# Kernel tuning notes

Hardware: AMD Instinct MI355X
Metric: run time of the kernel (lower is better)

## Reference

```python
import jax, jax.numpy as jnp
import numpy as np

B, T, C, H, D, K = 2, 2048, 1024, 16, 64, 4
INNER = H * D
EPS = 1e-6


def l2_norm(x):
    return x * jax.lax.rsqrt(jnp.sum(x * x, axis=-1, keepdims=True) + EPS)


def rms_norm(x):
    return x * jax.lax.rsqrt(jnp.mean(x * x, axis=-1, keepdims=True) + EPS)


def conv_silu(x, w, b):
    # causal depthwise conv1d + SiLU; x: [B,T,inner], w: [inner,1,K], b: [inner]
    xc = jnp.transpose(x, (0, 2, 1))
    xc = jnp.pad(xc, ((0, 0), (0, 0), (K - 1, 0)))
    xc = jax.lax.conv_general_dilated(
        xc, w.astype(xc.dtype), window_strides=(1,), padding='VALID',
        dimension_numbers=('NCW', 'OIW', 'NCW'), feature_group_count=xc.shape[1])
    xc = xc + b.astype(xc.dtype)[:, None]
    return jnp.transpose(jax.nn.silu(xc), (0, 2, 1))


def setup_inputs() -> dict:
    key = jax.random.key(0)
    ks = jax.random.split(key, 16)

    def lin(k, o, i):
        return jax.random.normal(k, (o, i), jnp.float32) / np.float32(np.sqrt(i))

    dt_min, dt_max = 0.001, 0.1
    dt = jnp.exp(jax.random.uniform(ks[12], (H,)) * (np.log(dt_max) - np.log(dt_min)) + np.log(dt_min))
    return {
        'x': jax.random.normal(ks[0], (B, T, C), jnp.float32),
        'wq': lin(ks[1], INNER, C), 'wk': lin(ks[2], INNER, C),
        'wv': lin(ks[3], INNER, C), 'wg': lin(ks[4], INNER, C),
        'wo': lin(ks[5], C, INNER),
        'wa': lin(ks[6], H, C), 'wb': lin(ks[7], H, C),
        'conv_q_w': jax.random.normal(ks[8], (INNER, 1, K)) * 0.02, 'conv_q_b': jnp.zeros(INNER),
        'conv_k_w': jax.random.normal(ks[9], (INNER, 1, K)) * 0.02, 'conv_k_b': jnp.zeros(INNER),
        'conv_v_w': jax.random.normal(ks[10], (INNER, 1, K)) * 0.02, 'conv_v_b': jnp.zeros(INNER),
        'A_log': jnp.log(jax.random.uniform(ks[11], (H,), minval=0.0, maxval=16.0) + 1e-6),
        'dt_bias': dt + jnp.log(-jnp.expm1(-dt)),
        'o_norm_scale': jnp.ones(D),
    }


def reference(x, wq, wk, wv, wg, wo, wa, wb,
              conv_q_w, conv_q_b, conv_k_w, conv_k_b, conv_v_w, conv_v_b,
              A_log, dt_bias, o_norm_scale):
    q = conv_silu(x @ wq.T, conv_q_w, conv_q_b).reshape(B, T, H, D)
    k = conv_silu(x @ wk.T, conv_k_w, conv_k_b).reshape(B, T, H, D)
    v = conv_silu(x @ wv.T, conv_v_w, conv_v_b).reshape(B, T, H, D)
    g_out = (x @ wg.T).reshape(B, T, H, D)

    q = l2_norm(q)
    k = l2_norm(k)

    beta = jax.nn.sigmoid(x @ wb.T)                     # [B,T,H]
    a = x @ wa.T + dt_bias                              # [B,T,H]
    decay = jnp.exp(-jnp.exp(A_log) * jax.nn.softplus(a))

    # time-major for scan
    q_T = jnp.transpose(q, (1, 0, 2, 3))
    k_T = jnp.transpose(k, (1, 0, 2, 3))
    v_T = jnp.transpose(v, (1, 0, 2, 3))
    beta_T = jnp.transpose(beta, (1, 0, 2))
    decay_T = jnp.transpose(decay, (1, 0, 2))

    def step(S_prev, xs):
        q_t, k_t, v_t, beta_t, decay_t = xs
        kS = jnp.einsum('bhd,bhde->bhe', k_t, S_prev)
        delta = v_t - kS
        write = beta_t[..., None, None] * jnp.einsum('bhd,bhe->bhde', k_t, delta)
        S_new = decay_t[..., None, None] * S_prev + write
        o_t = jnp.einsum('bhd,bhde->bhe', q_t, S_new)
        return S_new, o_t

    S_init = jnp.zeros((B, H, D, D), dtype=x.dtype)
    _, o_T = jax.lax.scan(step, S_init, (q_T, k_T, v_T, beta_T, decay_T))

    o = jnp.transpose(o_T, (1, 0, 2, 3))                # [B,T,H,D]
    o = rms_norm(o) * o_norm_scale
    o = o * jax.nn.silu(g_out)
    return o.reshape(B, T, INNER) @ wo.T
```

## Files before the change

### kernel.cpp

```cpp
#include <hip/hip_runtime.h>
#include <math.h>

#define BB 2
#define TT 2048
#define CC 1024
#define HH 16
#define DD 64
#define INNER 1024
#define BT (BB*TT)
#define EPSF 1e-6f
#define CH 64
#define NC (TT/CH)
#define NBH (BB*HH)
#define NCHK (NBH*NC)

typedef unsigned short u16;
typedef __bf16 bf16x8 __attribute__((ext_vector_type(8)));
typedef float f32x4 __attribute__((ext_vector_type(4)));

__device__ inline u16 f2bf(float f) {
  unsigned u = __builtin_bit_cast(unsigned, f);
  return (u16)((u + 0x7fffu + ((u >> 16) & 1u)) >> 16);
}
__device__ inline float b2f(u16 b) {
  unsigned u = ((unsigned)b) << 16;
  return __builtin_bit_cast(float, u);
}
__device__ inline void gll16(const u16* g, u16* l) {
  __builtin_amdgcn_global_load_lds(
      (const __attribute__((address_space(1))) void*)g,
      (__attribute__((address_space(3))) void*)l, 16, 0, 0);
}

__device__ u16   g_pqb[BT * INNER];
__device__ u16   g_pkb[BT * INNER];
__device__ u16   g_pvb[BT * INNER];
__device__ u16   g_qb [BT * INNER];
__device__ u16   g_kb [BT * INNER];
__device__ u16   g_vb [BT * INNER];
__device__ u16   g_gb [BT * INNER];
__device__ u16   g_ob [BT * INNER];
__device__ float g_beta[BT * HH];
__device__ float g_ldec[BT * HH];
__device__ u16   g_xb[BT * CC];
__device__ u16   g_wbb[4 * INNER * CC];
__device__ u16   g_wob[CC * INNER];
__device__ u16   g_gatedb[BT * INNER];
__device__ u16   g_U0 [NCHK * CH * DD];
__device__ u16   g_Wt [NCHK * DD * CH];
__device__ u16   g_Bt [NCHK * CH * CH];
__device__ u16   g_Qht[NCHK * DD * CH];
__device__ float g_Mc [NCHK * DD * DD];
__device__ float g_bc [NCHK * DD * DD];
__device__ float g_Sall[NCHK * DD * DD];

__global__ __launch_bounds__(256) void cast_all(
    const float* __restrict__ x, const float* __restrict__ wq,
    const float* __restrict__ wk, const float* __restrict__ wv,
    const float* __restrict__ wg, const float* __restrict__ wo,
    u16* __restrict__ xb, u16* __restrict__ wb, u16* __restrict__ wob) {
  long i = ((long)blockIdx.x * 256 + threadIdx.x) * 4;
  const float* src;
  u16* dst;
  if (i < 4194304)      { src = x  + i;             dst = xb + i; }
  else if (i < 5242880) { src = wq + (i - 4194304); dst = wb + (i - 4194304); }
  else if (i < 6291456) { src = wk + (i - 5242880); dst = wb + (i - 4194304); }
  else if (i < 7340032) { src = wv + (i - 6291456); dst = wb + (i - 4194304); }
  else if (i < 8388608) { src = wg + (i - 7340032); dst = wb + (i - 4194304); }
  else                  { src = wo + (i - 8388608); dst = wob + (i - 8388608); }
  float4 v = *(const float4*)src;
  ushort4 o;
  o.x = f2bf(v.x); o.y = f2bf(v.y); o.z = f2bf(v.z); o.w = f2bf(v.w);
  *(ushort4*)dst = o;
}

template <typename OutT, int NBN>
__global__ __launch_bounds__(256) void bgemm4(
    const u16* __restrict__ A, const u16* __restrict__ B,
    OutT* __restrict__ c0, OutT* __restrict__ c1,
    OutT* __restrict__ c2, OutT* __restrict__ c3) {
  __shared__ u16 lA[128 * 64];
  __shared__ u16 lB[128 * 64];
  const int tid = threadIdx.x;
  const int bid = blockIdx.x;
  int bm, bn;
  if constexpr (NBN == 32) {
    const int xcd = bid & 7;
    const int idx = bid >> 3;
    const int in_ = idx >> 4;
    int im = idx & 15;
    im = (in_ & 1) ? (15 - im) : im;
    bm = ((xcd >> 2) * 16 + im) * 128;
    bn = ((xcd & 3) * 8 + in_) * 128;
  } else {
    const int xcd = bid & 7;
    const int idx = bid >> 3;
    const int in_ = idx >> 2;
    int im = idx & 3;
    im = (in_ & 1) ? (3 - im) : im;
    bm = (xcd * 4 + im) * 128;
    bn = in_ * 128;
  }
  const int lane = tid & 63;
  const int wave = tid >> 6;
  const int wr = (wave >> 1) * 64, wc = (wave & 1) * 64;
  const int lr = lane & 15;
  const int kq = lane >> 4;
  const int srow0 = tid >> 3;
  const int gcol = ((tid & 7) ^ (srow0 & 7)) * 8;
  const u16* gA0 = &A[(long)(bm + srow0) * CC + gcol];
  const u16* gB0 = &B[(long)(bn + srow0) * CC + gcol];
  u16* lA0 = &lA[tid * 8];
  u16* lB0 = &lB[tid * 8];
  f32x4 acc[4][4] = {};

  for (int k0 = 0; k0 < CC; k0 += 64) {
    __syncthreads();
#pragma unroll
    for (int p = 0; p < 4; ++p) {
      gll16(gA0 + (long)p * 32 * CC + k0, lA0 + p * 2048);
      gll16(gB0 + (long)p * 32 * CC + k0, lB0 + p * 2048);
    }
    __syncthreads();
#pragma unroll
    for (int ks = 0; ks < 2; ++ks) {
      const int sl = ((ks * 4 + kq) ^ (lr & 7)) * 8;
      bf16x8 af[4], bf_[4];
#pragma unroll
      for (int m = 0; m < 4; ++m)
        af[m] = __builtin_bit_cast(bf16x8,
            *(const uint4*)&lA[(wr + m * 16 + lr) * 64 + sl]);
#pragma unroll
      for (int n = 0; n < 4; ++n)
        bf_[n] = __builtin_bit_cast(bf16x8,
            *(const uint4*)&lB[(wc + n * 16 + lr) * 64 + sl]);
#pragma unroll
      for (int m = 0; m < 4; ++m)
#pragma unroll
        for (int n = 0; n < 4; ++n)
          acc[m][n] = __builtin_amdgcn_mfma_f32_16x16x32_bf16(
              af[m], bf_[n], acc[m][n], 0, 0, 0);
    }
  }
  OutT* cp = (bn < 1024) ? c0 : (bn < 2048) ? c1 : (bn < 3072) ? c2 : c3;
  const int ccol0 = (bn & 1023) + wc;
  const int crow0 = bm + wr + kq * 4;
#pragma unroll
  for (int m = 0; m < 4; ++m)
#pragma unroll
    for (int n = 0; n < 4; ++n) {
      int col = ccol0 + n * 16 + lr;
#pragma unroll
      for (int r = 0; r < 4; ++r) {
        long idx2 = (long)(crow0 + m * 16 + r) * INNER + col;
        if constexpr (sizeof(OutT) == 2) cp[idx2] = f2bf(acc[m][n][r]);
        else                             cp[idx2] = acc[m][n][r];
      }
    }
}

__global__ __launch_bounds__(256) void conv3(
    const u16* __restrict__ pq, const u16* __restrict__ pk,
    const u16* __restrict__ pv,
    const float* __restrict__ cqw, const float* __restrict__ cqb,
    const float* __restrict__ ckw, const float* __restrict__ ckb,
    const float* __restrict__ cvw, const float* __restrict__ cvb,
    u16* __restrict__ oq, u16* __restrict__ ok, u16* __restrict__ ov) {
  const int which = blockIdx.y;
  const u16* pre = which == 0 ? pq : which == 1 ? pk : pv;
  const float* cw = which == 0 ? cqw : which == 1 ? ckw : cvw;
  const float* cb = which == 0 ? cqb : which == 1 ? ckb : cvb;
  u16* out = which == 0 ? oq : which == 1 ? ok : ov;
  const int do_l2 = (which < 2);

  const int bt = blockIdx.x;
  const int b = bt / TT, t = bt % TT;
  const int tid = threadIdx.x;
  const int c4 = tid * 4;
  float xt[4][4];
#pragma unroll
  for (int j = 0; j < 4; ++j) {
    int ts = t - 3 + j;
    if (ts >= 0) {
      ushort4 u = *(const ushort4*)&pre[(long)(b * TT + ts) * INNER + c4];
      xt[j][0] = b2f(u.x); xt[j][1] = b2f(u.y);
      xt[j][2] = b2f(u.z); xt[j][3] = b2f(u.w);
    } else {
      xt[j][0] = xt[j][1] = xt[j][2] = xt[j][3] = 0.f;
    }
  }
  float4 bias4 = *(const float4*)&cb[c4];
  const float* bp = (const float*)&bias4;
  float y[4];
#pragma unroll
  for (int ci = 0; ci < 4; ++ci) {
    float4 w4 = *(const float4*)&cw[(c4 + ci) * 4];
    float acc = bp[ci];
    acc += w4.x * xt[0][ci];
    acc += w4.y * xt[1][ci];
    acc += w4.z * xt[2][ci];
    acc += w4.w * xt[3][ci];
    y[ci] = acc / (1.f + expf(-acc));
  }
  if (do_l2) {
    float ssq = y[0]*y[0] + y[1]*y[1] + y[2]*y[2] + y[3]*y[3];
    ssq += __shfl_xor(ssq, 1);
    ssq += __shfl_xor(ssq, 2);
    ssq += __shfl_xor(ssq, 4);
    ssq += __shfl_xor(ssq, 8);
    float r = rsqrtf(ssq + EPSF);
    y[0] *= r; y[1] *= r; y[2] *= r; y[3] *= r;
  }
  ushort4 res;
  res.x = f2bf(y[0]); res.y = f2bf(y[1]);
  res.z = f2bf(y[2]); res.w = f2bf(y[3]);
  *(ushort4*)&out[(long)bt * INNER + c4] = res;
}

__global__ __launch_bounds__(256) void proj_ab3(
    const float* __restrict__ x, const float* __restrict__ wa,
    const float* __restrict__ wb, const float* __restrict__ dt_bias,
    const float* __restrict__ A_log, float* __restrict__ beta,
    float* __restrict__ ldec) {
  const int m0 = blockIdx.x * 8;
  const int tid = threadIdx.x;
  __shared__ float xs[8][132];
  __shared__ float ws[32][132];
  const int row = tid >> 5;
  const int col = tid & 31;
  float a0 = 0.f, a1 = 0.f, a2 = 0.f, a3 = 0.f;
  const int sxr = tid >> 5, sxc = (tid & 31) * 4;
  for (int k0 = 0; k0 < CC; k0 += 128) {
    __syncthreads();
    *(float4*)&xs[sxr][sxc] = *(const float4*)&x[(long)(m0 + sxr) * CC + k0 + sxc];
#pragma unroll
    for (int p = 0; p < 4; ++p) {
      int idx = tid + p * 256;
      int wr = idx >> 5, wc4 = (idx & 31) * 4;
      const float* wsrc = (wr < 16) ? &wa[(long)wr * CC] : &wb[(long)(wr - 16) * CC];
      *(float4*)&ws[wr][wc4] = *(const float4*)&wsrc[k0 + wc4];
    }
    __syncthreads();
#pragma unroll
    for (int kk = 0; kk < 128; kk += 16) {
      float4 x0 = *(const float4*)&xs[row][kk + 0];
      float4 w0 = *(const float4*)&ws[col][kk + 0];
      float4 x1 = *(const float4*)&xs[row][kk + 4];
      float4 w1 = *(const float4*)&ws[col][kk + 4];
      float4 x2 = *(const float4*)&xs[row][kk + 8];
      float4 w2 = *(const float4*)&ws[col][kk + 8];
      float4 x3 = *(const float4*)&xs[row][kk + 12];
      float4 w3 = *(const float4*)&ws[col][kk + 12];
      a0 += x0.x * w0.x + x0.y * w0.y + x0.z * w0.z + x0.w * w0.w;
      a1 += x1.x * w1.x + x1.y * w1.y + x1.z * w1.z + x1.w * w1.w;
      a2 += x2.x * w2.x + x2.y * w2.y + x2.z * w2.z + x2.w * w2.w;
      a3 += x3.x * w3.x + x3.y * w3.y + x3.z * w3.z + x3.w * w3.w;
    }
  }
  float acc = (a0 + a1) + (a2 + a3);
  const int m = m0 + row;
  if (col < 16) {
    float a = acc + dt_bias[col];
    float sp = fmaxf(a, 0.f) + log1pf(expf(-fabsf(a)));
    ldec[(long)m * HH + col] = -expf(A_log[col]) * sp;
  } else {
    beta[(long)m * HH + (col - 16)] = 1.f / (1.f + expf(-acc));
  }
}

__global__ __launch_bounds__(256) void gdn_prep(
    const u16* __restrict__ q, const u16* __restrict__ k,
    const u16* __restrict__ v, const float* __restrict__ beta,
    const float* __restrict__ ldec,
    u16* __restrict__ U0g, u16* __restrict__ Wtg, u16* __restrict__ Btg,
    u16* __restrict__ Qhtg, float* __restrict__ Mtg, float* __restrict__ bvg) {
  const int blk = blockIdx.x;
  const int bh = blk / NC, c = blk % NC;
  const int b = bh >> 4, h = bh & 15;
  const int tid = threadIdx.x;
  const int tx = tid & 15, ty = tid >> 4;
  __shared__ float P0[64][68];
  __shared__ float P1[64][68];
  __shared__ float Ab[64][68];
  __shared__ float lam[64], lamx[64], lbet[64];
  const long gb = ((long)(b * TT + c * CH) * HH + h) * DD;

  {
    const int e4 = (tid & 15) * 4;
    const int t0 = tid >> 4;
#pragma unroll
    for (int p = 0; p < 4; ++p) {
      int t = t0 + p * 16;
      ushort4 qv = *(const ushort4*)&q[gb + (long)t * (HH * DD) + e4];
      P1[e4 + 0][t] = b2f(qv.x); P1[e4 + 1][t] = b2f(qv.y);
      P1[e4 + 2][t] = b2f(qv.z); P1[e4 + 3][t] = b2f(qv.w);
    }
  }
  float ldv = 0.f, bv_ = 0.f;
  if (tid < 64) {
    ldv = ldec[(long)(b * TT + c * CH + tid) * HH + h];
    bv_ = beta[(long)(b * TT + c * CH + tid) * HH + h];
    lam[tid] = ldv;
  }
  __syncthreads();
  float lsum = 0.f;
  if (tid < 64) {
    for (int s = 0; s <= tid; ++s) lsum += lam[s];
  }
  __syncthreads();
  if (tid < 64) {
    lam[tid] = lsum;
    lamx[tid] = lsum - ldv;
    lbet[tid] = bv_;
  }
  __syncthreads();

  {
    const int lane = tid & 63;
    const int wave = tid >> 6;
    const int lr = lane & 15;
    const int kq = lane >> 4;
    const int mwr = (wave >> 1) * 32, mwc = (wave & 1) * 32;
    bf16x8 af[2][2], bk_[2][2], bq_[2][2];
#pragma unroll
    for (int m = 0; m < 2; ++m)
#pragma unroll
      for (int ks = 0; ks < 2; ++ks) {
        long rbase = gb + (long)(mwr + m * 16 + lr) * (HH * DD) + ks * 32 + kq * 8;
        long cbase = gb + (long)(mwc + m * 16 + lr) * (HH * DD) + ks * 32 + kq * 8;
        af[m][ks]  = __builtin_bit_cast(bf16x8, *(const uint4*)&k[rbase]);
        bk_[m][ks] = __builtin_bit_cast(bf16x8, *(const uint4*)&k[cbase]);
        bq_[m][ks] = __builtin_bit_cast(bf16x8, *(const uint4*)&q[cbase]);
      }
    f32x4 gf[2][2] = {}, pf[2][2] = {};
#pragma unroll
    for (int ks = 0; ks < 2; ++ks)
#pragma unroll
      for (int m = 0; m < 2; ++m)
#pragma unroll
        for (int n = 0; n < 2; ++n) {
          gf[m][n] = __builtin_amdgcn_mfma_f32_16x16x32_bf16(
              af[m][ks], bk_[n][ks], gf[m][n], 0, 0, 0);
          pf[m][n] = __builtin_amdgcn_mfma_f32_16x16x32_bf16(
              af[m][ks], bq_[n][ks], pf[m][n], 0, 0, 0);
        }
    u16* btp = Btg + (long)blk * (CH * CH);
#pragma unroll
    for (int m = 0; m < 2; ++m)
#pragma unroll
      for (int n = 0; n < 2; ++n)
#pragma unroll
        for (int r = 0; r < 4; ++r) {
          int t = mwr + m * 16 + kq * 4 + r;
          int s = mwc + n * 16 + lr;
          Ab[t][s] = (s < t) ? lbet[t] * expf(lamx[t] - lam[s]) * gf[m][n][r]
                             : 0.f;
          btp[t * 64 + s] = f2bf(
              (t <= s) ? expf(lam[s] - lam[t]) * pf[m][n][r] : 0.f);
        }
  }
  {
    u16* qhp = Qhtg + (long)blk * (DD * CH);
    const int t4 = (tid & 15) * 4;
    const int d0 = tid >> 4;
#pragma unroll
    for (int p = 0; p < 4; ++p) {
      int d = d0 + p * 16;
      float4 qv = *(const float4*)&P1[d][t4];
      ushort4 qw;
      qw.x = f2bf(qv.x * expf(lam[t4 + 0]));
      qw.y = f2bf(qv.y * expf(lam[t4 + 1]));
      qw.z = f2bf(qv.z * expf(lam[t4 + 2]));
      qw.w = f2bf(qv.w * expf(lam[t4 + 3]));
      *(ushort4*)&qhp[d * 64 + t4] = qw;
    }
  }
  __syncthreads();
  {
    const int e4 = (tid & 15) * 4;
    const int t0 = tid >> 4;
#pragma unroll
    for (int p = 0; p < 4; ++p) {
      int t = t0 + p * 16;
      float bt_ = lbet[t], cx = bt_ * expf(lamx[t]);
      ushort4 vv4 = *(const ushort4*)&v[gb + (long)t * (HH * DD) + e4];
      ushort4 kv4 = *(const ushort4*)&k[gb + (long)t * (HH * DD) + e4];
      float4 vv = make_float4(b2f(vv4.x) * bt_, b2f(vv4.y) * bt_,
                              b2f(vv4.z) * bt_, b2f(vv4.w) * bt_);
      float4 kv = make_float4(b2f(kv4.x) * cx, b2f(kv4.y) * cx,
                              b2f(kv4.z) * cx, b2f(kv4.w) * cx);
      *(float4*)&P0[t][e4] = vv;
      *(float4*)&P1[t][e4] = kv;
    }
  }
  __syncthreads();
  {
    const int i = tid >> 5;
    const int j4 = (tid & 31) * 4;
    float* Pj = (j4 < 64) ? (&P0[0][0] + j4) : (&P1[0][0] + (j4 - 64));
#pragma unroll
    for (int base = 0; base < 64; base += 8) {
      const int r = base + i;
      float4 acc = *(const float4*)&Pj[r * 68];
      for (int t = 0; t < base; ++t) {
        float a = Ab[r][t];
        float4 ut = *(const float4*)&Pj[t * 68];
        acc.x -= a * ut.x; acc.y -= a * ut.y;
        acc.z -= a * ut.z; acc.w -= a * ut.w;
      }
      *(float4*)&Pj[r * 68] = acc;
      __syncthreads();
      float4 val[8];
#pragma unroll
      for (int t = 0; t < 8; ++t) {
        float4 vt = *(const float4*)&Pj[(base + t) * 68];
#pragma unroll
        for (int m = 0; m < t; ++m) {
          float a = Ab[base + t][base + m];
          vt.x -= a * val[m].x; vt.y -= a * val[m].y;
          vt.z -= a * val[m].z; vt.w -= a * val[m].w;
        }
        val[t] = vt;
      }
      float4 fin = val[0];
#pragma unroll
      for (int t = 1; t < 8; ++t) if (i == t) fin = val[t];
      __syncthreads();
      *(float4*)&Pj[r * 68] = fin;
      __syncthreads();
    }
  }
  {
    u16* u0p = U0g + (long)blk * (CH * DD);
    const int e4 = (tid & 15) * 4;
    const int t0 = tid >> 4;
    float lamL = lam[63];
#pragma unroll
    for (int p = 0; p < 4; ++p) {
      int t = t0 + p * 16;
      float4 u4 = *(const float4*)&P0[t][e4];
      ushort4 uw;
      uw.x = f2bf(u4.x); uw.y = f2bf(u4.y);
      uw.z = f2bf(u4.z); uw.w = f2bf(u4.w);
      *(ushort4*)&u0p[t * 64 + e4] = uw;
      float cf = expf(lamL - lam[t]);
      ushort4 kv4 = *(const ushort4*)&k[gb + (long)t * (HH * DD) + e4];
      *(float4*)&Ab[t][e4] = make_float4(b2f(kv4.x) * cf, b2f(kv4.y) * cf,
                                         b2f(kv4.z) * cf, b2f(kv4.w) * cf);
    }
    u16* wtp = Wtg + (long)blk * (DD * CH);
    const int t = tid & 63;
    const int d0 = tid >> 6;
#pragma unroll
    for (int p = 0; p < 16; ++p) {
      int d = d0 + p * 4;
      wtp[d * 64 + t] = f2bf(P1[t][d]);
    }
  }
  __syncthreads();
  {
    float accm[4][4] = {}, accb[4][4] = {};
    for (int t = 0; t < 64; ++t) {
      float4 ka = *(const float4*)&Ab[t][ty * 4];
      float4 wc_ = *(const float4*)&P1[t][tx * 4];
      float4 uv = *(const float4*)&P0[t][tx * 4];
      float kar[4] = {ka.x, ka.y, ka.z, ka.w};
      float wcr[4] = {wc_.x, wc_.y, wc_.z, wc_.w};
      float ucr[4] = {uv.x, uv.y, uv.z, uv.w};
#pragma unroll
      for (int i = 0; i < 4; ++i)
#pragma unroll
        for (int j = 0; j < 4; ++j) {
          accm[i][j] += kar[i] * wcr[j];
          accb[i][j] += kar[i] * ucr[j];
        }
    }
    float gLv = expf(lam[63]);
    float* mp = Mtg + (long)blk * (DD * DD);
    float* bp = bvg + (long)blk * (DD * DD);
#pragma unroll
    for (int i = 0; i < 4; ++i) {
      int rr = ty * 4 + i;
      float4 mv, b4;
      mv.x = ((rr == tx * 4 + 0) ? gLv : 0.f) - accm[i][0];
      mv.y = ((rr == tx * 4 + 1) ? gLv : 0.f) - accm[i][1];
      mv.z = ((rr == tx * 4 + 2) ? gLv : 0.f) - accm[i][2];
      mv.w = ((rr == tx * 4 + 3) ? gLv : 0.f) - accm[i][3];
      *(float4*)&mp[rr * 64 + tx * 4] = mv;
      b4.x = accb[i][0]; b4.y = accb[i][1];
      b4.z = accb[i][2]; b4.w = accb[i][3];
      *(float4*)&bp[rr * 64 + tx * 4] = b4;
    }
  }
}

__global__ __launch_bounds__(256) void gdn_seq5(
    const float* __restrict__ Mtg, const float* __restrict__ bvg,
    float* __restrict__ Sall) {
  const int bh = blockIdx.x & 31;
  const int esec = blockIdx.x >> 5;
  const int tid = threadIdx.x;
  const int lane = tid & 63;
  const int w = tid >> 6;
  const int d = w * 16 + (lane & 15);
  const int q = lane >> 4;
  const int eo = esec * 4;
  __shared__ float Ss[4][68];
  float S0 = 0.f, S1 = 0.f, S2 = 0.f, S3 = 0.f;
  float4 mreg[4], mnext[4];
  float4 breg, bnext;
  {
    const float* mt0 = Mtg + (long)bh * NC * 4096;
#pragma unroll
    for (int p = 0; p < 4; ++p)
      mreg[p] = *(const float4*)&mt0[d * 64 + q * 16 + p * 4];
    breg = *(const float4*)&bvg[(long)bh * NC * 4096 + d * 64 + eo];
  }
  for (int c = 0; c < NC; ++c) {
    const long cb = (long)bh * NC + c;
    if (q == 0) {
      *(float4*)&Sall[cb * 4096 + d * 64 + eo] = make_float4(S0, S1, S2, S3);
      Ss[0][d] = S0; Ss[1][d] = S1; Ss[2][d] = S2; Ss[3][d] = S3;
    }
    __syncthreads();
    if (c + 1 < NC) {
      const float* mtn = Mtg + (cb + 1) * 4096;
#pragma unroll
      for (int p = 0; p < 4; ++p)
        mnext[p] = *(const float4*)&mtn[d * 64 + q * 16 + p * 4];
      bnext = *(const float4*)&bvg[(cb + 1) * 4096 + d * 64 + eo];
    }
    float p0 = 0.f, p1 = 0.f, p2 = 0.f, p3 = 0.f;
#pragma unroll
    for (int j = 0; j < 4; ++j) {
      float4 m4 = mreg[j];
      float4 s0 = *(const float4*)&Ss[0][q * 16 + j * 4];
      float4 s1 = *(const float4*)&Ss[1][q * 16 + j * 4];
      float4 s2 = *(const float4*)&Ss[2][q * 16 + j * 4];
      float4 s3 = *(const float4*)&Ss[3][q * 16 + j * 4];
      p0 += m4.x * s0.x + m4.y * s0.y + m4.z * s0.z + m4.w * s0.w;
      p1 += m4.x * s1.x + m4.y * s1.y + m4.z * s1.z + m4.w * s1.w;
      p2 += m4.x * s2.x + m4.y * s2.y + m4.z * s2.z + m4.w * s2.w;
      p3 += m4.x * s3.x + m4.y * s3.y + m4.z * s3.z + m4.w * s3.w;
    }
    p0 += __shfl_xor(p0, 16); p0 += __shfl_xor(p0, 32);
    p1 += __shfl_xor(p1, 16); p1 += __shfl_xor(p1, 32);
    p2 += __shfl_xor(p2, 16); p2 += __shfl_xor(p2, 32);
    p3 += __shfl_xor(p3, 16); p3 += __shfl_xor(p3, 32);
    S0 = breg.x + p0; S1 = breg.y + p1;
    S2 = breg.z + p2; S3 = breg.w + p3;
    __syncthreads();
    mreg[0] = mnext[0]; mreg[1] = mnext[1];
    mreg[2] = mnext[2]; mreg[3] = mnext[3];
    breg = bnext;
  }
}

__global__ __launch_bounds__(256) void gdn_out(
    const u16* __restrict__ U0g, const u16* __restrict__ Wtg,
    const u16* __restrict__ Btg, const u16* __restrict__ Qhtg,
    const float* __restrict__ Sall, u16* __restrict__ o) {
  const int blk = blockIdx.x;
  const int bh = blk / NC, c = blk % NC;
  const int b = bh >> 4, h = bh & 15;
  const int tid = threadIdx.x;
  const int tx = tid & 15, ty = tid >> 4;
  __shared__ float S[64][64];
  __shared__ float ub[64][64];
  __shared__ float op[64][64];
  const int e4 = (tid & 15) * 4;
  const int t0s = tid >> 4;
  {
    const int r = tid >> 2, qq = (tid & 3) * 16;
#pragma unroll
    for (int p = 0; p < 4; ++p)
      *(float4*)&S[r][qq + p * 4] =
          *(const float4*)&Sall[(long)blk * 4096 + r * 64 + qq + p * 4];
  }
#pragma unroll
  for (int p = 0; p < 4; ++p) {
    int t = t0s + p * 16;
    ushort4 w4 = *(const ushort4*)&Wtg[(long)blk * 4096 + t * 64 + e4];
    *(float4*)&op[t][e4] = make_float4(b2f(w4.x), b2f(w4.y), b2f(w4.z), b2f(w4.w));
  }
  __syncthreads();
  float acc[4][4];
#pragma unroll
  for (int i = 0; i < 4; ++i) {
    ushort4 u4 = *(const ushort4*)&U0g[(long)blk * 4096 + (ty * 4 + i) * 64 + tx * 4];
    acc[i][0] = b2f(u4.x); acc[i][1] = b2f(u4.y);
    acc[i][2] = b2f(u4.z); acc[i][3] = b2f(u4.w);
  }
  for (int d = 0; d < 64; ++d) {
    float4 a4 = *(const float4*)&op[d][ty * 4];
    float4 b4 = *(const float4*)&S[d][tx * 4];
    float ar[4] = {a4.x, a4.y, a4.z, a4.w};
    float br[4] = {b4.x, b4.y, b4.z, b4.w};
#pragma unroll
    for (int i = 0; i < 4; ++i)
#pragma unroll
      for (int j = 0; j < 4; ++j) acc[i][j] -= ar[i] * br[j];
  }
#pragma unroll
  for (int i = 0; i < 4; ++i)
    *(float4*)&ub[ty * 4 + i][tx * 4] =
        make_float4(acc[i][0], acc[i][1], acc[i][2], acc[i][3]);
  __syncthreads();
#pragma unroll
  for (int p = 0; p < 4; ++p) {
    int t = t0s + p * 16;
    ushort4 w4 = *(const ushort4*)&Btg[(long)blk * 4096 + t * 64 + e4];
    *(float4*)&op[t][e4] = make_float4(b2f(w4.x), b2f(w4.y), b2f(w4.z), b2f(w4.w));
  }
  __syncthreads();
  float acco[4][4] = {};
  for (int s = 0; s < 64; ++s) {
    float4 a4 = *(const float4*)&op[s][ty * 4];
    float4 b4 = *(const float4*)&ub[s][tx * 4];
    float ar[4] = {a4.x, a4.y, a4.z, a4.w};
    float br[4] = {b4.x, b4.y, b4.z, b4.w};
#pragma unroll
    for (int i = 0; i < 4; ++i)
#pragma unroll
      for (int j = 0; j < 4; ++j) acco[i][j] += ar[i] * br[j];
  }
  __syncthreads();
#pragma unroll
  for (int p = 0; p < 4; ++p) {
    int t = t0s + p * 16;
    ushort4 w4 = *(const ushort4*)&Qhtg[(long)blk * 4096 + t * 64 + e4];
    *(float4*)&op[t][e4] = make_float4(b2f(w4.x), b2f(w4.y), b2f(w4.z), b2f(w4.w));
  }
  __syncthreads();
  for (int d = 0; d < 64; ++d) {
    float4 a4 = *(const float4*)&op[d][ty * 4];
    float4 b4 = *(const float4*)&S[d][tx * 4];
    float ar[4] = {a4.x, a4.y, a4.z, a4.w};
    float br[4] = {b4.x, b4.y, b4.z, b4.w};
#pragma unroll
    for (int i = 0; i < 4; ++i)
#pragma unroll
      for (int j = 0; j < 4; ++j) acco[i][j] += ar[i] * br[j];
  }
#pragma unroll
  for (int i = 0; i < 4; ++i) {
    int t = ty * 4 + i;
    ushort4 ow;
    ow.x = f2bf(acco[i][0]); ow.y = f2bf(acco[i][1]);
    ow.z = f2bf(acco[i][2]); ow.w = f2bf(acco[i][3]);
    *(ushort4*)&o[((long)(b * TT + c * CH + t) * HH + h) * DD + tx * 4] = ow;
  }
}

__global__ __launch_bounds__(256) void norm_gate(
    const u16* __restrict__ o, const u16* __restrict__ g,
    const float* __restrict__ scale, u16* __restrict__ outb) {
  const int bt = blockIdx.x;
  const int tid = threadIdx.x;
  const int c4 = tid * 4;
  ushort4 o4u = *(const ushort4*)&o[(long)bt * INNER + c4];
  float4 o4 = make_float4(b2f(o4u.x), b2f(o4u.y), b2f(o4u.z), b2f(o4u.w));
  float ssq = o4.x * o4.x + o4.y * o4.y + o4.z * o4.z + o4.w * o4.w;
  ssq += __shfl_xor(ssq, 1);
  ssq += __shfl_xor(ssq, 2);
  ssq += __shfl_xor(ssq, 4);
  ssq += __shfl_xor(ssq, 8);
  float r = rsqrtf(ssq * (1.f / 64.f) + EPSF);
  float4 sc = *(const float4*)&scale[c4 & 63];
  ushort4 g4u = *(const ushort4*)&g[(long)bt * INNER + c4];
  float4 g4 = make_float4(b2f(g4u.x), b2f(g4u.y), b2f(g4u.z), b2f(g4u.w));
  ushort4 res;
  res.x = f2bf(o4.x * r * sc.x * (g4.x / (1.f + expf(-g4.x))));
  res.y = f2bf(o4.y * r * sc.y * (g4.y / (1.f + expf(-g4.y))));
  res.z = f2bf(o4.z * r * sc.z * (g4.z / (1.f + expf(-g4.z))));
  res.w = f2bf(o4.w * r * sc.w * (g4.w / (1.f + expf(-g4.w))));
  *(ushort4*)&outb[(long)bt * INNER + c4] = res;
}

extern "C" void kernel_launch(void* const* d_in, const int* in_sizes, int n_in,
                              void* d_out, int out_size, void* d_ws,
                              size_t ws_size, hipStream_t stream) {
  const float* x      = (const float*)d_in[0];
  const float* wq     = (const float*)d_in[1];
  const float* wk     = (const float*)d_in[2];
  const float* wv     = (const float*)d_in[3];
  const float* wg     = (const float*)d_in[4];
  const float* wo     = (const float*)d_in[5];
  const float* wa     = (const float*)d_in[6];
  const float* wb     = (const float*)d_in[7];
  const float* cqw    = (const float*)d_in[8];
  const float* cqb    = (const float*)d_in[9];
  const float* ckw    = (const float*)d_in[10];
  const float* ckb    = (const float*)d_in[11];
  const float* cvw    = (const float*)d_in[12];
  const float* cvb    = (const float*)d_in[13];
  const float* A_log  = (const float*)d_in[14];
  const float* dtb    = (const float*)d_in[15];
  const float* oscale = (const float*)d_in[16];
  float* out = (float*)d_out;

  u16 *pqb, *pkb, *pvb, *qb, *kb, *vb, *gb, *ob;
  u16 *xb, *wbb, *wob, *gatedb, *U0, *Wt, *Bt, *Qht;
  float *beta, *ldec, *Mc, *bc, *Sall;
  hipGetSymbolAddress((void**)&pqb,   HIP_SYMBOL(g_pqb));
  hipGetSymbolAddress((void**)&pkb,   HIP_SYMBOL(g_pkb));
  hipGetSymbolAddress((void**)&pvb,   HIP_SYMBOL(g_pvb));
  hipGetSymbolAddress((void**)&qb,    HIP_SYMBOL(g_qb));
  hipGetSymbolAddress((void**)&kb,    HIP_SYMBOL(g_kb));
  hipGetSymbolAddress((void**)&vb,    HIP_SYMBOL(g_vb));
  hipGetSymbolAddress((void**)&gb,    HIP_SYMBOL(g_gb));
  hipGetSymbolAddress((void**)&ob,    HIP_SYMBOL(g_ob));
  hipGetSymbolAddress((void**)&beta,  HIP_SYMBOL(g_beta));
  hipGetSymbolAddress((void**)&ldec,  HIP_SYMBOL(g_ldec));
  hipGetSymbolAddress((void**)&xb,    HIP_SYMBOL(g_xb));
  hipGetSymbolAddress((void**)&wbb,   HIP_SYMBOL(g_wbb));
  hipGetSymbolAddress((void**)&wob,   HIP_SYMBOL(g_wob));
  hipGetSymbolAddress((void**)&gatedb,HIP_SYMBOL(g_gatedb));
  hipGetSymbolAddress((void**)&U0,    HIP_SYMBOL(g_U0));
  hipGetSymbolAddress((void**)&Wt,    HIP_SYMBOL(g_Wt));
  hipGetSymbolAddress((void**)&Bt,    HIP_SYMBOL(g_Bt));
  hipGetSymbolAddress((void**)&Qht,   HIP_SYMBOL(g_Qht));
  hipGetSymbolAddress((void**)&Mc,    HIP_SYMBOL(g_Mc));
  hipGetSymbolAddress((void**)&bc,    HIP_SYMBOL(g_bc));
  hipGetSymbolAddress((void**)&Sall,  HIP_SYMBOL(g_Sall));

  cast_all<<<9216, 256, 0, stream>>>(x, wq, wk, wv, wg, wo, xb, wbb, wob);

  bgemm4<u16, 32><<<1024, 256, 0, stream>>>(xb, wbb, pqb, pkb, pvb, gb);

  conv3<<<dim3(BT, 3), 256, 0, stream>>>(pqb, pkb, pvb,
                                         cqw, cqb, ckw, ckb, cvw, cvb,
                                         qb, kb, vb);
  proj_ab3<<<BT / 8, 256, 0, stream>>>(x, wa, wb, dtb, A_log, beta, ldec);

  gdn_prep<<<NCHK, 256, 0, stream>>>(qb, kb, vb, beta, ldec,
                                     U0, Wt, Bt, Qht, Mc, bc);
  gdn_seq5<<<NBH * 16, 256, 0, stream>>>(Mc, bc, Sall);
  gdn_out<<<NCHK, 256, 0, stream>>>(U0, Wt, Bt, Qht, Sall, ob);

  norm_gate<<<BT, 256, 0, stream>>>(ob, gb, oscale, gatedb);

  bgemm4<float, 8><<<256, 256, 0, stream>>>(gatedb, wob, out, out, out, out);
}
```

Before: 273.7 us.

## Fuse RMS-norm and SiLU gate into gdn_out; widen triangular solve blocks

```diff
diff --git a/kernel.cpp b/kernel.cpp
--- a/kernel.cpp
+++ b/kernel.cpp
@@ -39,7 +39,6 @@
 __device__ u16   g_kb [BT * INNER];
 __device__ u16   g_vb [BT * INNER];
 __device__ u16   g_gb [BT * INNER];
-__device__ u16   g_ob [BT * INNER];
 __device__ float g_beta[BT * HH];
 __device__ float g_ldec[BT * HH];
 __device__ u16   g_xb[BT * CC];
@@ -399,20 +398,24 @@
     const int j4 = (tid & 31) * 4;
     float* Pj = (j4 < 64) ? (&P0[0][0] + j4) : (&P1[0][0] + (j4 - 64));
 #pragma unroll
-    for (int base = 0; base < 64; base += 8) {
-      const int r = base + i;
-      float4 acc = *(const float4*)&Pj[r * 68];
+    for (int base = 0; base < 64; base += 16) {
+      const int r0 = base + i, r1 = base + i + 8;
+      float4 a0 = *(const float4*)&Pj[r0 * 68];
+      float4 a1 = *(const float4*)&Pj[r1 * 68];
       for (int t = 0; t < base; ++t) {
-        float a = Ab[r][t];
+        float c0 = Ab[r0][t], c1 = Ab[r1][t];
         float4 ut = *(const float4*)&Pj[t * 68];
-        acc.x -= a * ut.x; acc.y -= a * ut.y;
-        acc.z -= a * ut.z; acc.w -= a * ut.w;
+        a0.x -= c0 * ut.x; a0.y -= c0 * ut.y;
+        a0.z -= c0 * ut.z; a0.w -= c0 * ut.w;
+        a1.x -= c1 * ut.x; a1.y -= c1 * ut.y;
+        a1.z -= c1 * ut.z; a1.w -= c1 * ut.w;
       }
-      *(float4*)&Pj[r * 68] = acc;
+      *(float4*)&Pj[r0 * 68] = a0;
+      *(float4*)&Pj[r1 * 68] = a1;
       __syncthreads();
-      float4 val[8];
-#pragma unroll
-      for (int t = 0; t < 8; ++t) {
+      float4 val[16];
+#pragma unroll
+      for (int t = 0; t < 16; ++t) {
         float4 vt = *(const float4*)&Pj[(base + t) * 68];
 #pragma unroll
         for (int m = 0; m < t; ++m) {
@@ -422,11 +425,13 @@
         }
         val[t] = vt;
       }
-      float4 fin = val[0];
-#pragma unroll
-      for (int t = 1; t < 8; ++t) if (i == t) fin = val[t];
+      float4 f0 = val[0], f1 = val[8];
+#pragma unroll
+      for (int t = 1; t < 8; ++t)
+        if (i == t) { f0 = val[t]; f1 = val[t + 8]; }
       __syncthreads();
-      *(float4*)&Pj[r * 68] = fin;
+      *(float4*)&Pj[r0 * 68] = f0;
+      *(float4*)&Pj[r1 * 68] = f1;
       __syncthreads();
     }
   }
@@ -559,7 +564,8 @@
 __global__ __launch_bounds__(256) void gdn_out(
     const u16* __restrict__ U0g, const u16* __restrict__ Wtg,
     const u16* __restrict__ Btg, const u16* __restrict__ Qhtg,
-    const float* __restrict__ Sall, u16* __restrict__ o) {
+    const float* __restrict__ Sall, const u16* __restrict__ gg,
+    const float* __restrict__ scale, u16* __restrict__ gated) {
   const int blk = blockIdx.x;
   const int bh = blk / NC, c = blk % NC;
   const int b = bh >> 4, h = bh & 15;
@@ -642,39 +648,27 @@
 #pragma unroll
       for (int j = 0; j < 4; ++j) acco[i][j] += ar[i] * br[j];
   }
+  float4 sc = *(const float4*)&scale[tx * 4];
 #pragma unroll
   for (int i = 0; i < 4; ++i) {
     int t = ty * 4 + i;
-    ushort4 ow;
-    ow.x = f2bf(acco[i][0]); ow.y = f2bf(acco[i][1]);
-    ow.z = f2bf(acco[i][2]); ow.w = f2bf(acco[i][3]);
-    *(ushort4*)&o[((long)(b * TT + c * CH + t) * HH + h) * DD + tx * 4] = ow;
-  }
-}
-
-__global__ __launch_bounds__(256) void norm_gate(
-    const u16* __restrict__ o, const u16* __restrict__ g,
-    const float* __restrict__ scale, u16* __restrict__ outb) {
-  const int bt = blockIdx.x;
-  const int tid = threadIdx.x;
-  const int c4 = tid * 4;
-  ushort4 o4u = *(const ushort4*)&o[(long)bt * INNER + c4];
-  float4 o4 = make_float4(b2f(o4u.x), b2f(o4u.y), b2f(o4u.z), b2f(o4u.w));
-  float ssq = o4.x * o4.x + o4.y * o4.y + o4.z * o4.z + o4.w * o4.w;
-  ssq += __shfl_xor(ssq, 1);
-  ssq += __shfl_xor(ssq, 2);
-  ssq += __shfl_xor(ssq, 4);
-  ssq += __shfl_xor(ssq, 8);
-  float r = rsqrtf(ssq * (1.f / 64.f) + EPSF);
-  float4 sc = *(const float4*)&scale[c4 & 63];
-  ushort4 g4u = *(const ushort4*)&g[(long)bt * INNER + c4];
-  float4 g4 = make_float4(b2f(g4u.x), b2f(g4u.y), b2f(g4u.z), b2f(g4u.w));
-  ushort4 res;
-  res.x = f2bf(o4.x * r * sc.x * (g4.x / (1.f + expf(-g4.x))));
-  res.y = f2bf(o4.y * r * sc.y * (g4.y / (1.f + expf(-g4.y))));
-  res.z = f2bf(o4.z * r * sc.z * (g4.z / (1.f + expf(-g4.z))));
-  res.w = f2bf(o4.w * r * sc.w * (g4.w / (1.f + expf(-g4.w))));
-  *(ushort4*)&outb[(long)bt * INNER + c4] = res;
+    float ssq = acco[i][0] * acco[i][0] + acco[i][1] * acco[i][1] +
+                acco[i][2] * acco[i][2] + acco[i][3] * acco[i][3];
+    ssq += __shfl_xor(ssq, 1);
+    ssq += __shfl_xor(ssq, 2);
+    ssq += __shfl_xor(ssq, 4);
+    ssq += __shfl_xor(ssq, 8);
+    float r = rsqrtf(ssq * (1.f / 64.f) + EPSF);
+    long gidx = ((long)(b * TT + c * CH + t) * HH + h) * DD + tx * 4;
+    ushort4 g4u = *(const ushort4*)&gg[gidx];
+    float4 g4 = make_float4(b2f(g4u.x), b2f(g4u.y), b2f(g4u.z), b2f(g4u.w));
+    ushort4 res;
+    res.x = f2bf(acco[i][0] * r * sc.x * (g4.x / (1.f + expf(-g4.x))));
+    res.y = f2bf(acco[i][1] * r * sc.y * (g4.y / (1.f + expf(-g4.y))));
+    res.z = f2bf(acco[i][2] * r * sc.z * (g4.z / (1.f + expf(-g4.z))));
+    res.w = f2bf(acco[i][3] * r * sc.w * (g4.w / (1.f + expf(-g4.w))));
+    *(ushort4*)&gated[gidx] = res;
+  }
 }
 
 extern "C" void kernel_launch(void* const* d_in, const int* in_sizes, int n_in,
@@ -699,7 +693,7 @@
   const float* oscale = (const float*)d_in[16];
   float* out = (float*)d_out;
 
-  u16 *pqb, *pkb, *pvb, *qb, *kb, *vb, *gb, *ob;
+  u16 *pqb, *pkb, *pvb, *qb, *kb, *vb, *gb;
   u16 *xb, *wbb, *wob, *gatedb, *U0, *Wt, *Bt, *Qht;
   float *beta, *ldec, *Mc, *bc, *Sall;
   hipGetSymbolAddress((void**)&pqb,   HIP_SYMBOL(g_pqb));
@@ -709,7 +703,6 @@
   hipGetSymbolAddress((void**)&kb,    HIP_SYMBOL(g_kb));
   hipGetSymbolAddress((void**)&vb,    HIP_SYMBOL(g_vb));
   hipGetSymbolAddress((void**)&gb,    HIP_SYMBOL(g_gb));
-  hipGetSymbolAddress((void**)&ob,    HIP_SYMBOL(g_ob));
   hipGetSymbolAddress((void**)&beta,  HIP_SYMBOL(g_beta));
   hipGetSymbolAddress((void**)&ldec,  HIP_SYMBOL(g_ldec));
   hipGetSymbolAddress((void**)&xb,    HIP_SYMBOL(g_xb));
@@ -736,9 +729,7 @@
   gdn_prep<<<NCHK, 256, 0, stream>>>(qb, kb, vb, beta, ldec,
                                      U0, Wt, Bt, Qht, Mc, bc);
   gdn_seq5<<<NBH * 16, 256, 0, stream>>>(Mc, bc, Sall);
-  gdn_out<<<NCHK, 256, 0, stream>>>(U0, Wt, Bt, Qht, Sall, ob);
-
-  norm_gate<<<BT, 256, 0, stream>>>(ob, gb, oscale, gatedb);
+  gdn_out<<<NCHK, 256, 0, stream>>>(U0, Wt, Bt, Qht, Sall, gb, oscale, gatedb);
 
   bgemm4<float, 8><<<256, 256, 0, stream>>>(gatedb, wob, out, out, out, out);
 }
```

Result: no change. 270.3 us (-1.2%).
